# Optimization experiments

Hardware: AMD Instinct MI355X
Metric: run time of the kernel (lower is better)

Reference implementation:

```python
import jax, jax.numpy as jnp
import numpy as np

N_NODES = 20000
N_EDGES = 320000
DIM = 256
OUT_DIM = 256
N_LAYERS = 2
AVG_LOG = float(np.log(17.0))  # PNA avg_deg['log'] from deg histogram (all degree 16)
STD_EPS = 1e-5
N_AGG = 5
N_SCALER = 3


def _pna_conv(x, edge_index, Wpre, bpre, Wpost, bpost, Wlin, blin):
    """PyG PNAConv (towers=1, pre_layers=1, post_layers=1, divide_input=False)."""
    N = x.shape[0]
    src, dst = edge_index[0], edge_index[1]  # messages flow src -> dst
    # pre_nn on concat([x_i, x_j]) per edge: [E, 2F] -> [E, F]
    m = jnp.concatenate([x[dst], x[src]], axis=-1) @ Wpre.T + bpre
    deg = jax.ops.segment_sum(jnp.ones((src.shape[0],), x.dtype), dst, num_segments=N)
    degc = jnp.maximum(deg, 1.0)[:, None]
    s = jax.ops.segment_sum(m, dst, num_segments=N)
    mean = s / degc
    mean2 = jax.ops.segment_sum(m * m, dst, num_segments=N) / degc
    std = jnp.sqrt(jax.nn.relu(mean2 - mean * mean) + STD_EPS)
    has = (deg > 0)[:, None]
    mn = jnp.where(has, jax.ops.segment_min(m, dst, num_segments=N), 0.0)
    mx = jnp.where(has, jax.ops.segment_max(m, dst, num_segments=N), 0.0)
    agg = jnp.concatenate([mean, s, std, mn, mx], axis=-1)  # [N, 5F]
    logd = jnp.log(degc + 1.0)
    scaled = jnp.concatenate(
        [agg, agg * (logd / AVG_LOG), agg * (AVG_LOG / logd)], axis=-1)  # [N, 15F]
    h = jnp.concatenate([x, scaled], axis=-1) @ Wpost.T + bpost  # [N, F_out]
    return h @ Wlin.T + blin


def setup_inputs() -> dict:
    key = jax.random.key(0)
    ks = jax.random.split(key, 20)
    F = DIM
    L = N_LAYERS
    post_in = (N_AGG * N_SCALER + 1) * F  # 16F = 4096
    sc = 0.05
    inp = {
        "x": jax.random.normal(ks[0], (N_NODES, F), jnp.float32),
        "edge_index_in": jax.random.randint(ks[1], (2, N_EDGES), 0, N_NODES),
        "edge_index_out": jax.random.randint(ks[2], (2, N_EDGES), 0, N_NODES),
    }
    def p(k, shape):
        return sc * jax.random.normal(k, shape, jnp.float32)
    # stacked per-layer params; supply (_s) and demand (_d) channels
    for tag, base in (("s", 3), ("d", 9)):
        inp[f"Wpre_{tag}"] = p(ks[base + 0], (L, F, 2 * F))
        inp[f"bpre_{tag}"] = p(ks[base + 1], (L, F))
        inp[f"Wpost_{tag}"] = p(ks[base + 2], (L, OUT_DIM, post_in))
        inp[f"bpost_{tag}"] = p(ks[base + 3], (L, OUT_DIM))
        inp[f"Wlin_{tag}"] = p(ks[base + 4], (L, OUT_DIM, OUT_DIM))
        inp[f"blin_{tag}"] = p(ks[base + 5], (L, OUT_DIM))
    inp["Wcomb"] = p(ks[15], (L, OUT_DIM, F + 2 * OUT_DIM))
    inp["bcomb"] = p(ks[16], (L, OUT_DIM))
    inp["Wout"] = p(ks[17], (1, OUT_DIM))
    inp["bout"] = p(ks[18], (1,))
    return inp


def reference(x, edge_index_in, edge_index_out,
              Wpre_s, bpre_s, Wpost_s, bpost_s, Wlin_s, blin_s,
              Wpre_d, bpre_d, Wpost_d, bpost_d, Wlin_d, blin_d,
              Wcomb, bcomb, Wout, bout):
    for l in range(N_LAYERS):
        h_in = jax.nn.relu(_pna_conv(x, edge_index_in,
                                     Wpre_s[l], bpre_s[l], Wpost_s[l], bpost_s[l],
                                     Wlin_s[l], blin_s[l]))
        h_out = jax.nn.relu(_pna_conv(x, edge_index_out,
                                      Wpre_d[l], bpre_d[l], Wpost_d[l], bpost_d[l],
                                      Wlin_d[l], blin_d[l]))
        x = jax.nn.relu(jnp.concatenate([x, h_in, h_out], axis=-1) @ Wcomb[l].T + bcomb[l])
    return jnp.squeeze(x @ Wout.T + bout)  # [N]
```

## Files before the change

### kernel.cpp

```cpp
#include <hip/hip_runtime.h>
#include <math.h>

#define NN 20000
#define NE 320000
#define AVG_LOG_F 2.83321334f

typedef unsigned short u16;
typedef _Float16 h8_t __attribute__((ext_vector_type(8)));
typedef float f4_t __attribute__((ext_vector_type(4)));

__device__ __forceinline__ u16 f2h(float f) {
  _Float16 h = (_Float16)f;
  return __builtin_bit_cast(u16, h);
}
__device__ __forceinline__ void gld16(const void* g, void* l) {
  __builtin_amdgcn_global_load_lds(
      (const __attribute__((address_space(1))) void*)g,
      (__attribute__((address_space(3))) void*)l, 16, 0, 0);
}

__global__ __launch_bounds__(256) void k_count2(const int* __restrict__ ein,
                                                const int* __restrict__ eout,
                                                int* __restrict__ deg2, int E) {
  int e = blockIdx.x * 256 + threadIdx.x;
  int ch = blockIdx.y;
  const int* dst = (ch ? eout : ein) + E;
  if (e < E) atomicAdd(&deg2[ch * NN + dst[e]], 1);
}

__global__ __launch_bounds__(1024) void k_scan(const int* __restrict__ deg,
                                               int* __restrict__ rp, int N) {
  __shared__ int lds[1024];
  int t = threadIdx.x;
  int CH = (N + 1023) >> 10;
  int base = t * CH;
  int s = 0;
  for (int i = 0; i < CH; ++i) { int idx = base + i; if (idx < N) s += deg[idx]; }
  lds[t] = s;
  __syncthreads();
  for (int off = 1; off < 1024; off <<= 1) {
    int v = (t >= off) ? lds[t - off] : 0;
    __syncthreads();
    lds[t] += v;
    __syncthreads();
  }
  int run = (t == 0) ? 0 : lds[t - 1];
  for (int i = 0; i < CH; ++i) {
    int idx = base + i;
    if (idx < N) { rp[idx] = run; run += deg[idx]; }
  }
  if (t == 1023) rp[N] = run;
}

__global__ __launch_bounds__(256) void k_scatter2(const int* __restrict__ ein,
                                                  const int* __restrict__ eout,
                                                  const int* __restrict__ rp2,
                                                  int* __restrict__ cur2,
                                                  int* __restrict__ col2, int E) {
  int e = blockIdx.x * 256 + threadIdx.x;
  int ch = blockIdx.y;
  const int* src = (ch ? eout : ein);
  const int* dst = src + E;
  if (e < E) {
    int d = dst[e];
    int p = atomicAdd(&cur2[ch * NN + d], 1);
    col2[rp2[ch * NN + d] + p] = src[e];
  }
}

__global__ __launch_bounds__(256) void k_cvtw(
    const float* __restrict__ Wpre_s, const float* __restrict__ Wpre_d,
    const float* __restrict__ Wlin_s, const float* __restrict__ Wlin_d,
    const float* __restrict__ Wcomb,
    u16* __restrict__ pre2, u16* __restrict__ lincat, u16* __restrict__ combB) {
  int i = blockIdx.x * 256 + threadIdx.x;
  const float* src;
  u16* dst;
  int so, dofs;
  if (i < 65536)       { int j = i; int lyr = j >> 15;
                         src = Wpre_s; dst = pre2; so = j;
                         dofs = (lyr * 2 + 0) * 32768 + (j & 32767); }
  else if (i < 131072) { int j = i - 65536; int lyr = j >> 15;
                         src = Wpre_d; dst = pre2; so = j;
                         dofs = (lyr * 2 + 1) * 32768 + (j & 32767); }
  else if (i < 163840) { int j = i - 131072; int lyr = j >> 14;
                         src = Wlin_s; dst = lincat; so = j; dofs = j + lyr * 16384; }
  else if (i < 196608) { int j = i - 163840; int lyr = j >> 14;
                         src = Wlin_d; dst = lincat; so = j; dofs = j + (lyr + 1) * 16384; }
  else if (i < 294912) { src = Wcomb; dst = combB; so = i - 196608; dofs = so; }
  else return;
  float4 v = *(const float4*)(src + (size_t)so * 4);
  ushort4 o;
  o.x = f2h(v.x); o.y = f2h(v.y); o.z = f2h(v.z); o.w = f2h(v.w);
  *(ushort4*)(dst + (size_t)dofs * 4) = o;
}

__global__ __launch_bounds__(256) void k_cvtx(const float* __restrict__ x,
                                              u16* __restrict__ xc,
                                              const float* __restrict__ bpre_s,
                                              const float* __restrict__ bpre_d,
                                              float* __restrict__ bpre4) {
  int i = blockIdx.x * 256 + threadIdx.x;
  int row = i >> 6, c = (i & 63) * 4;
  float4 v = *(const float4*)(x + (size_t)row * 256 + c);
  ushort4 o;
  o.x = f2h(v.x); o.y = f2h(v.y); o.z = f2h(v.z); o.w = f2h(v.w);
  *(ushort4*)(xc + (size_t)row * 768 + c) = o;
  if (i < 1024) {
    int z = i >> 8, n = i & 255;
    int lyr = z >> 1, ch = z & 1;
    bpre4[i] = (ch ? bpre_d : bpre_s)[lyr * 256 + n];
  }
}

__global__ __launch_bounds__(256) void k_tc4(const float* __restrict__ Ws,
                                             const float* __restrict__ Wd,
                                             u16* __restrict__ outT) {
  __shared__ float tile[32][33];
  int z = blockIdx.z;
  const float* in = ((z & 1) ? Wd : Ws) + (size_t)(z >> 1) * 256 * 4096;
  u16* out = outT + (size_t)z * (4096 * 256);
  int bx = blockIdx.x, by = blockIdx.y;
  int r = threadIdx.x >> 5, c = threadIdx.x & 31;
#pragma unroll
  for (int it = 0; it < 4; ++it)
    tile[r + it * 8][c] = in[(size_t)(by * 32 + r + it * 8) * 4096 + bx * 32 + c];
  __syncthreads();
#pragma unroll
  for (int it = 0; it < 4; ++it)
    out[(size_t)(bx * 32 + r + it * 8) * 256 + by * 32 + c] = f2h(tile[c][r + it * 8]);
}

__global__ __launch_bounds__(512) void k_mgemm(
    const u16* __restrict__ A, int lda,
    const u16* __restrict__ B, const u16* __restrict__ B2, int ldb, int nsplit,
    const float* __restrict__ bias, int zBias,
    u16* __restrict__ oH, int ldoH,
    int M, int K, int relu, int zA, int zB, int zO) {
  __shared__ u16 As[2][64 * 64];
  __shared__ u16 Bs[2][256 * 64];
  const int t = threadIdx.x;
  const int z = blockIdx.z;
  A += (size_t)z * zA;
  B += (size_t)z * zB;
  B2 += (size_t)z * zB;
  oH += (size_t)z * zO;
  if (bias) bias += (size_t)z * zBias;
  const int m0 = blockIdx.y * 64;
  const int n0 = blockIdx.x * 256;
  const int l = t & 63, w = t >> 6;
  const int wm = w >> 2, wn = w & 3;
  const int lo = l & 15, hi = l >> 4;

  f4_t acc[2][4];
#pragma unroll
  for (int i = 0; i < 2; ++i)
#pragma unroll
    for (int j = 0; j < 4; ++j) acc[i][j] = (f4_t)0.f;

  const int ra = t >> 3, pa = t & 7;
  const int la = pa ^ (ra & 7);
  int rra = m0 + ra;
  if (rra > M - 1) rra = M - 1;
  const u16* gA = A + (size_t)rra * lda + la * 8;

  const u16* gB[4];
  int lBo[4];
#pragma unroll
  for (int i = 0; i < 4; ++i) {
    int q = i * 512 + t;
    int r = q >> 3, p2 = q & 7;
    int lc = p2 ^ (r & 7);
    int n = n0 + r;
    const u16* bp = (n < nsplit) ? (B + (size_t)n * ldb) : (B2 + (size_t)(n - nsplit) * ldb);
    gB[i] = bp + lc * 8;
    lBo[i] = q * 8;
  }

  gld16(gA, &As[0][t * 8]);
#pragma unroll
  for (int i = 0; i < 4; ++i) gld16(gB[i], &Bs[0][lBo[i]]);
  __syncthreads();

  const int nt = K >> 6;
  for (int tt = 0; tt < nt; ++tt) {
    const int cur = tt & 1;
    if (tt + 1 < nt) {
      const int ko = (tt + 1) << 6;
      gld16(gA + ko, &As[cur ^ 1][t * 8]);
#pragma unroll
      for (int i = 0; i < 4; ++i) gld16(gB[i] + ko, &Bs[cur ^ 1][lBo[i]]);
    }
#pragma unroll
    for (int ks = 0; ks < 2; ++ks) {
      h8_t af[2], bfr[4];
#pragma unroll
      for (int mi = 0; mi < 2; ++mi) {
        int row = wm * 32 + mi * 16 + lo;
        int c = (ks * 4 + hi) ^ (row & 7);
        af[mi] = *(const h8_t*)&As[cur][row * 64 + c * 8];
      }
#pragma unroll
      for (int ni = 0; ni < 4; ++ni) {
        int row = wn * 64 + ni * 16 + lo;
        int c = (ks * 4 + hi) ^ (row & 7);
        bfr[ni] = *(const h8_t*)&Bs[cur][row * 64 + c * 8];
      }
#pragma unroll
      for (int mi = 0; mi < 2; ++mi)
#pragma unroll
        for (int ni = 0; ni < 4; ++ni)
          acc[mi][ni] = __builtin_amdgcn_mfma_f32_16x16x32_f16(
              af[mi], bfr[ni], acc[mi][ni], 0, 0, 0);
    }
    __syncthreads();
  }

  float bv[4];
#pragma unroll
  for (int ni = 0; ni < 4; ++ni) {
    int n = n0 + wn * 64 + ni * 16 + lo;
    bv[ni] = (n < nsplit) ? (bias ? bias[n] : 0.f) : 0.f;
  }
#pragma unroll
  for (int mi = 0; mi < 2; ++mi) {
#pragma unroll
    for (int r = 0; r < 4; ++r) {
      int m = m0 + wm * 32 + mi * 16 + hi * 4 + r;
      if (m < M) {
#pragma unroll
        for (int ni = 0; ni < 4; ++ni) {
          int n = n0 + wn * 64 + ni * 16 + lo;
          float v = acc[mi][ni][r] + bv[ni];
          if (relu && v < 0.f) v = 0.f;
          oH[(size_t)m * ldoH + n] = f2h(v);
        }
      }
    }
  }
}

__global__ __launch_bounds__(512) void k_pgemm(
    const u16* __restrict__ xc, const u16* __restrict__ agg5c,
    const float* __restrict__ scal3c, const u16* __restrict__ Wfl,
    const float* __restrict__ bfl, u16* __restrict__ oHb, int M) {
  __shared__ u16 As[64 * 64];
  __shared__ u16 Bs[256 * 64];
  const int t = threadIdx.x;
  const int ch = blockIdx.y;
  const u16* agg5 = agg5c + (size_t)ch * NN * 1280;
  const float* scal3 = scal3c + (size_t)ch * NN * 4;
  const u16* Wf = Wfl + (size_t)ch * (256 * 4096);
  const float* bf = bfl + ch * 256;
  u16* oH = oHb + 256 + ch * 256;
  const int m0 = blockIdx.x * 64;
  const int l = t & 63, w = t >> 6;
  const int wm = w >> 2, wn = w & 3;
  const int lo = l & 15, hi = l >> 4;

  f4_t acc[2][4];
#pragma unroll
  for (int i = 0; i < 2; ++i)
#pragma unroll
    for (int j = 0; j < 4; ++j) acc[i][j] = (f4_t)0.f;

  const int ra = t >> 3, pa = t & 7;
  int m = m0 + ra;
  if (m > M - 1) m = M - 1;
  u16* ldA = &As[ra * 64 + (pa ^ (ra & 7)) * 8];
  const u16* xrow = xc + (size_t)m * 768;
  const u16* arow = agg5 + (size_t)m * 1280;
  const float* srow = scal3 + (size_t)m * 4;

  const u16* gB[4];
  u16* lB[4];
#pragma unroll
  for (int i = 0; i < 4; ++i) {
    int q = i * 512 + t;
    int r = q >> 3, p2 = q & 7;
    int lc = p2 ^ (r & 7);
    gB[i] = Wf + (size_t)r * 4096 + lc * 8;
    lB[i] = &Bs[q * 8];
  }

  for (int k0 = 0; k0 < 4096; k0 += 64) {
#pragma unroll
    for (int i = 0; i < 4; ++i) gld16(gB[i] + k0, lB[i]);
    int k = k0 + pa * 8;
    h8_t v;
    if (k < 256) {
      v = *(const h8_t*)(xrow + k);
    } else {
      int q = k - 256;
      int g = q / 1280;
      int r2 = q - g * 1280;
      v = *(const h8_t*)(arow + r2);
      v = v * (_Float16)srow[g];
    }
    *(h8_t*)ldA = v;
    __syncthreads();
#pragma unroll
    for (int ks = 0; ks < 2; ++ks) {
      h8_t af[2], bfr[4];
#pragma unroll
      for (int mi = 0; mi < 2; ++mi) {
        int row = wm * 32 + mi * 16 + lo;
        int c = (ks * 4 + hi) ^ (row & 7);
        af[mi] = *(const h8_t*)&As[row * 64 + c * 8];
      }
#pragma unroll
      for (int ni = 0; ni < 4; ++ni) {
        int row = wn * 64 + ni * 16 + lo;
        int c = (ks * 4 + hi) ^ (row & 7);
        bfr[ni] = *(const h8_t*)&Bs[row * 64 + c * 8];
      }
#pragma unroll
      for (int mi = 0; mi < 2; ++mi)
#pragma unroll
        for (int ni = 0; ni < 4; ++ni)
          acc[mi][ni] = __builtin_amdgcn_mfma_f32_16x16x32_f16(
              af[mi], bfr[ni], acc[mi][ni], 0, 0, 0);
    }
    __syncthreads();
  }

  float bv[4];
#pragma unroll
  for (int ni = 0; ni < 4; ++ni) bv[ni] = bf[wn * 64 + ni * 16 + lo];
#pragma unroll
  for (int mi = 0; mi < 2; ++mi) {
#pragma unroll
    for (int r = 0; r < 4; ++r) {
      int mr = m0 + wm * 32 + mi * 16 + hi * 4 + r;
      if (mr < M) {
#pragma unroll
        for (int ni = 0; ni < 4; ++ni) {
          int n = wn * 64 + ni * 16 + lo;
          float vv = acc[mi][ni][r] + bv[ni];
          if (vv < 0.f) vv = 0.f;
          oH[(size_t)mr * 768 + n] = f2h(vv);
        }
      }
    }
  }
}

__global__ __launch_bounds__(256) void k_aggregate(
    const u16* __restrict__ AB2, const int* __restrict__ rp2,
    const int* __restrict__ col2, u16* __restrict__ agg52,
    float* __restrict__ scal32) {
  int ch = blockIdx.y;
  const u16* AB = AB2 + (size_t)ch * NN * 512;
  const int* rp = rp2 + ch * NN;
  u16* agg5 = agg52 + (size_t)ch * NN * 1280;
  float* scal3 = scal32 + (size_t)ch * NN * 4;
  int w = threadIdx.x >> 6, l = threadIdx.x & 63;
  int n = blockIdx.x * 4 + w;
  int beg = rp[n], end = rp[n + 1];
  int deg = end - beg;
  int half = l >> 5, lf = l & 31;
  float sb[8], qb[8], mnb[8], mxb[8];
#pragma unroll
  for (int j = 0; j < 8; ++j) {
    sb[j] = 0.f; qb[j] = 0.f;
    mnb[j] = 3.402823466e38f; mxb[j] = -3.402823466e38f;
  }
  for (int i = beg + half; i < end; i += 2) {
    int s = col2[i];
    h8_t bv = *(const h8_t*)(AB + (size_t)s * 512 + 256 + lf * 8);
#pragma unroll
    for (int j = 0; j < 8; ++j) {
      float b = (float)bv[j];
      sb[j] += b;
      qb[j] = fmaf(b, b, qb[j]);
      mnb[j] = fminf(mnb[j], b);
      mxb[j] = fmaxf(mxb[j], b);
    }
  }
#pragma unroll
  for (int j = 0; j < 8; ++j) {
    sb[j] += __shfl_xor(sb[j], 32, 64);
    qb[j] += __shfl_xor(qb[j], 32, 64);
    mnb[j] = fminf(mnb[j], __shfl_xor(mnb[j], 32, 64));
    mxb[j] = fmaxf(mxb[j], __shfl_xor(mxb[j], 32, 64));
  }
  h8_t cv = *(const h8_t*)(AB + (size_t)n * 512 + lf * 8);
  float degf = (float)deg;
  float degc = degf > 1.f ? degf : 1.f;
  float inv = 1.f / degc;
  float ov[5][8];
#pragma unroll
  for (int j = 0; j < 8; ++j) {
    float c = (float)cv[j];
    float s_m = fmaf(degf, c, sb[j]);
    float mean = s_m * inv;
    float mean2 = fmaf(degf * c, c, fmaf(2.f * c, sb[j], qb[j])) * inv;
    float var = mean2 - mean * mean;
    if (var < 0.f) var = 0.f;
    float sd = sqrtf(var + 1e-5f);
    ov[0][j] = mean;
    ov[1][j] = s_m;
    ov[2][j] = sd;
    ov[3][j] = deg > 0 ? c + mnb[j] : 0.f;
    ov[4][j] = deg > 0 ? c + mxb[j] : 0.f;
  }
  if (half == 0) {
    u16* base = agg5 + (size_t)n * 1280 + lf * 8;
#pragma unroll
    for (int a = 0; a < 5; ++a) {
      h8_t o;
#pragma unroll
      for (int j = 0; j < 8; ++j) o[j] = (_Float16)ov[a][j];
      *(h8_t*)(base + a * 256) = o;
    }
    if (lf == 0) {
      float logd = logf(degc + 1.f);
      float4 sc = make_float4(1.f, logd / AVG_LOG_F, AVG_LOG_F / logd, 0.f);
      *(float4*)(scal3 + (size_t)n * 4) = sc;
    }
  }
}

__global__ __launch_bounds__(256) void k_bfuse4(
    const float* __restrict__ Wlin_s, const float* __restrict__ Wlin_d,
    const float* __restrict__ bpost_s, const float* __restrict__ bpost_d,
    const float* __restrict__ blin_s, const float* __restrict__ blin_d,
    float* __restrict__ bfv4) {
  __shared__ float bp[256];
  int z = blockIdx.x, lyr = z >> 1, ch = z & 1;
  const float* Wlin = (ch ? Wlin_d : Wlin_s) + (size_t)lyr * 65536;
  const float* bpost = (ch ? bpost_d : bpost_s) + lyr * 256;
  const float* blin = (ch ? blin_d : blin_s) + lyr * 256;
  int t = threadIdx.x;
  bp[t] = bpost[t];
  __syncthreads();
  float s = blin[t];
  for (int k = 0; k < 256; ++k) s = fmaf(Wlin[t * 256 + k], bp[k], s);
  bfv4[z * 256 + t] = s;
}

__global__ __launch_bounds__(256) void k_wout(const u16* __restrict__ x,
                                              const float* __restrict__ w,
                                              const float* __restrict__ b,
                                              float* __restrict__ out, int N) {
  int wid = threadIdx.x >> 6, lane = threadIdx.x & 63;
  int n = blockIdx.x * 4 + wid;
  if (n >= N) return;
  ushort4 xv = *(const ushort4*)(x + (size_t)n * 256 + lane * 4);
  const float4 wv = *(const float4*)(w + lane * 4);
  float s = (float)__builtin_bit_cast(_Float16, xv.x) * wv.x +
            (float)__builtin_bit_cast(_Float16, xv.y) * wv.y +
            (float)__builtin_bit_cast(_Float16, xv.z) * wv.z +
            (float)__builtin_bit_cast(_Float16, xv.w) * wv.w;
#pragma unroll
  for (int off = 32; off > 0; off >>= 1) s += __shfl_down(s, off);
  if (lane == 0) out[n] = s + b[0];
}

extern "C" void kernel_launch(void* const* d_in, const int* in_sizes, int n_in,
                              void* d_out, int out_size, void* d_ws, size_t ws_size,
                              hipStream_t stream) {
  const float* x0      = (const float*)d_in[0];
  const int*   ei_in   = (const int*)d_in[1];
  const int*   ei_out  = (const int*)d_in[2];
  const float* Wpre_s  = (const float*)d_in[3];
  const float* bpre_s  = (const float*)d_in[4];
  const float* Wpost_s = (const float*)d_in[5];
  const float* bpost_s = (const float*)d_in[6];
  const float* Wlin_s  = (const float*)d_in[7];
  const float* blin_s  = (const float*)d_in[8];
  const float* Wpre_d  = (const float*)d_in[9];
  const float* bpre_d  = (const float*)d_in[10];
  const float* Wpost_d = (const float*)d_in[11];
  const float* bpost_d = (const float*)d_in[12];
  const float* Wlin_d  = (const float*)d_in[13];
  const float* blin_d  = (const float*)d_in[14];
  const float* Wcomb   = (const float*)d_in[15];
  const float* bcomb   = (const float*)d_in[16];
  const float* Wout    = (const float*)d_in[17];
  const float* bout    = (const float*)d_in[18];
  float* out = (float*)d_out;

  char* p = (char*)d_ws;
  auto alloc = [&](size_t b) {
    char* r = p;
    p += (b + 255) & ~(size_t)255;
    return r;
  };
  int* deg2     = (int*)alloc((size_t)2 * NN * 4);
  int* cur2     = (int*)alloc((size_t)2 * NN * 4);
  int* rp2      = (int*)alloc((size_t)(2 * NN + 1) * 4);
  int* col2     = (int*)alloc((size_t)2 * NE * 4);
  u16* AB2      = (u16*)alloc((size_t)2 * NN * 512 * 2);
  u16* agg52    = (u16*)alloc((size_t)2 * NN * 1280 * 2);
  float* scal32 = (float*)alloc((size_t)2 * NN * 4 * 4);
  u16* xcat1    = (u16*)alloc((size_t)NN * 768 * 2);
  u16* xcat2    = (u16*)alloc((size_t)NN * 768 * 2);
  u16* pre2     = (u16*)alloc((size_t)4 * 256 * 512 * 2);
  u16* lincat   = (u16*)alloc((size_t)4 * 256 * 256 * 2);
  u16* combB    = (u16*)alloc((size_t)2 * 256 * 768 * 2);
  u16* Wf4      = (u16*)alloc((size_t)4 * 256 * 4096 * 2);
  float* bfv4   = (float*)alloc((size_t)4 * 256 * 4);
  float* bpre4  = (float*)alloc((size_t)4 * 256 * 4);
  u16* WpostT4  = (u16*)agg52;
  u16* xfin     = xcat1;

  const int BIG = 1 << 30;

  k_cvtw<<<1152, 256, 0, stream>>>(Wpre_s, Wpre_d, Wlin_s, Wlin_d, Wcomb,
                                   pre2, lincat, combB);
  k_cvtx<<<5000, 256, 0, stream>>>(x0, xcat1, bpre_s, bpre_d, bpre4);
  hipMemsetAsync(deg2, 0, (size_t)4 * NN * 4, stream);
  k_count2<<<dim3(1250, 2), 256, 0, stream>>>(ei_in, ei_out, deg2, NE);
  k_scan<<<1, 1024, 0, stream>>>(deg2, rp2, 2 * NN);
  k_scatter2<<<dim3(1250, 2), 256, 0, stream>>>(ei_in, ei_out, rp2, cur2, col2, NE);
  k_tc4<<<dim3(128, 8, 4), 256, 0, stream>>>(Wpost_s, Wpost_d, WpostT4);
  k_mgemm<<<dim3(16, 4, 4), 512, 0, stream>>>(
      lincat, 256, WpostT4, WpostT4, 256, BIG, nullptr, 0,
      Wf4, 4096, 256, 256, 0, 65536, 1048576, 1048576);
  k_bfuse4<<<4, 256, 0, stream>>>(Wlin_s, Wlin_d, bpost_s, bpost_d, blin_s, blin_d, bfv4);

  u16* xcs[2] = {xcat1, xcat2};
  for (int lyr = 0; lyr < 2; ++lyr) {
    u16* xc = xcs[lyr];
    k_mgemm<<<dim3(2, 313, 2), 512, 0, stream>>>(
        xc, 768, pre2 + (size_t)lyr * 2 * 131072, pre2 + (size_t)lyr * 2 * 131072 + 256,
        512, 256, bpre4 + (size_t)lyr * 2 * 256, 256,
        AB2, 512, NN, 256, 0, 0, 131072, NN * 512);
    k_aggregate<<<dim3(5000, 2), 256, 0, stream>>>(AB2, rp2, col2, agg52, scal32);
    k_pgemm<<<dim3(313, 2), 512, 0, stream>>>(
        xc, agg52, scal32, Wf4 + (size_t)lyr * 2 * 1048576, bfv4 + lyr * 512, xc, NN);
    if (lyr == 0) {
      k_mgemm<<<dim3(1, 313, 1), 512, 0, stream>>>(
          xc, 768, combB, combB, 768, BIG, bcomb, 0,
          xcat2, 768, NN, 768, 1, 0, 0, 0);
    } else {
      k_mgemm<<<dim3(1, 313, 1), 512, 0, stream>>>(
          xc, 768, combB + 196608, combB + 196608, 768, BIG, bcomb + 256, 0,
          xfin, 256, NN, 768, 1, 0, 0, 0);
    }
  }
  k_wout<<<5000, 256, 0, stream>>>(xfin, Wout, bout, out, NN);
}
```

Measured before the change: 807.9 us.

## Double pgemm M-tile to 128 rows and remap blocks by XCD for channel locality

The post-aggregation GEMM now computes 128-row tiles instead of 64, so each 256x64 weight tile loaded into LDS is reused across twice as many rows, halving weight traffic per output. The grid is flattened to 320 blocks and the block index is decoded so that blocks on the same XCD (wg&7) share a channel and adjacent M-tiles, aiming to improve L2 reuse of that channel's weights. This costs double the accumulator registers and larger LDS, which may lower occupancy, and leaves fewer blocks (314 active) to fill the GPU.

```diff
diff --git a/kernel.cpp b/kernel.cpp
--- a/kernel.cpp
+++ b/kernel.cpp
@@ -244,33 +244,43 @@
     const u16* __restrict__ xc, const u16* __restrict__ agg5c,
     const float* __restrict__ scal3c, const u16* __restrict__ Wfl,
     const float* __restrict__ bfl, u16* __restrict__ oHb, int M) {
-  __shared__ u16 As[64 * 64];
+  __shared__ u16 As[128 * 64];
   __shared__ u16 Bs[256 * 64];
   const int t = threadIdx.x;
-  const int ch = blockIdx.y;
+  const int wg = blockIdx.x;
+  const int xcd = wg & 7;
+  const int ch = xcd >> 2;
+  const int mt = (wg >> 3) * 4 + (xcd & 3);
+  if (mt >= 157) return;
+  const int m0 = mt * 128;
   const u16* agg5 = agg5c + (size_t)ch * NN * 1280;
   const float* scal3 = scal3c + (size_t)ch * NN * 4;
   const u16* Wf = Wfl + (size_t)ch * (256 * 4096);
   const float* bf = bfl + ch * 256;
   u16* oH = oHb + 256 + ch * 256;
-  const int m0 = blockIdx.x * 64;
   const int l = t & 63, w = t >> 6;
   const int wm = w >> 2, wn = w & 3;
   const int lo = l & 15, hi = l >> 4;
 
-  f4_t acc[2][4];
-#pragma unroll
-  for (int i = 0; i < 2; ++i)
+  f4_t acc[4][4];
+#pragma unroll
+  for (int i = 0; i < 4; ++i)
 #pragma unroll
     for (int j = 0; j < 4; ++j) acc[i][j] = (f4_t)0.f;
 
   const int ra = t >> 3, pa = t & 7;
-  int m = m0 + ra;
-  if (m > M - 1) m = M - 1;
-  u16* ldA = &As[ra * 64 + (pa ^ (ra & 7)) * 8];
-  const u16* xrow = xc + (size_t)m * 768;
-  const u16* arow = agg5 + (size_t)m * 1280;
-  const float* srow = scal3 + (size_t)m * 4;
+  int mr0 = m0 + ra;
+  if (mr0 > M - 1) mr0 = M - 1;
+  int mr1 = m0 + ra + 64;
+  if (mr1 > M - 1) mr1 = M - 1;
+  u16* ldA0 = &As[ra * 64 + (pa ^ (ra & 7)) * 8];
+  u16* ldA1 = ldA0 + 64 * 64;
+  const u16* xrow0 = xc + (size_t)mr0 * 768;
+  const u16* xrow1 = xc + (size_t)mr1 * 768;
+  const u16* arow0 = agg5 + (size_t)mr0 * 1280;
+  const u16* arow1 = agg5 + (size_t)mr1 * 1280;
+  const float* srow0 = scal3 + (size_t)mr0 * 4;
+  const float* srow1 = scal3 + (size_t)mr1 * 4;
 
   const u16* gB[4];
   u16* lB[4];
@@ -287,24 +297,28 @@
 #pragma unroll
     for (int i = 0; i < 4; ++i) gld16(gB[i] + k0, lB[i]);
     int k = k0 + pa * 8;
-    h8_t v;
+    h8_t v0, v1;
     if (k < 256) {
-      v = *(const h8_t*)(xrow + k);
+      v0 = *(const h8_t*)(xrow0 + k);
+      v1 = *(const h8_t*)(xrow1 + k);
     } else {
       int q = k - 256;
       int g = q / 1280;
       int r2 = q - g * 1280;
-      v = *(const h8_t*)(arow + r2);
-      v = v * (_Float16)srow[g];
-    }
-    *(h8_t*)ldA = v;
+      v0 = *(const h8_t*)(arow0 + r2);
+      v1 = *(const h8_t*)(arow1 + r2);
+      v0 = v0 * (_Float16)srow0[g];
+      v1 = v1 * (_Float16)srow1[g];
+    }
+    *(h8_t*)ldA0 = v0;
+    *(h8_t*)ldA1 = v1;
     __syncthreads();
 #pragma unroll
     for (int ks = 0; ks < 2; ++ks) {
-      h8_t af[2], bfr[4];
-#pragma unroll
-      for (int mi = 0; mi < 2; ++mi) {
-        int row = wm * 32 + mi * 16 + lo;
+      h8_t af[4], bfr[4];
+#pragma unroll
+      for (int mi = 0; mi < 4; ++mi) {
+        int row = wm * 64 + mi * 16 + lo;
         int c = (ks * 4 + hi) ^ (row & 7);
         af[mi] = *(const h8_t*)&As[row * 64 + c * 8];
       }
@@ -315,7 +329,7 @@
         bfr[ni] = *(const h8_t*)&Bs[row * 64 + c * 8];
       }
 #pragma unroll
-      for (int mi = 0; mi < 2; ++mi)
+      for (int mi = 0; mi < 4; ++mi)
 #pragma unroll
         for (int ni = 0; ni < 4; ++ni)
           acc[mi][ni] = __builtin_amdgcn_mfma_f32_16x16x32_f16(
@@ -328,10 +342,10 @@
 #pragma unroll
   for (int ni = 0; ni < 4; ++ni) bv[ni] = bf[wn * 64 + ni * 16 + lo];
 #pragma unroll
-  for (int mi = 0; mi < 2; ++mi) {
+  for (int mi = 0; mi < 4; ++mi) {
 #pragma unroll
     for (int r = 0; r < 4; ++r) {
-      int mr = m0 + wm * 32 + mi * 16 + hi * 4 + r;
+      int mr = m0 + wm * 64 + mi * 16 + hi * 4 + r;
       if (mr < M) {
 #pragma unroll
         for (int ni = 0; ni < 4; ++ni) {
@@ -528,7 +542,7 @@
         512, 256, bpre4 + (size_t)lyr * 2 * 256, 256,
         AB2, 512, NN, 256, 0, 0, 131072, NN * 512);
     k_aggregate<<<dim3(5000, 2), 256, 0, stream>>>(AB2, rp2, col2, agg52, scal32);
-    k_pgemm<<<dim3(313, 2), 512, 0, stream>>>(
+    k_pgemm<<<320, 512, 0, stream>>>(
         xc, agg52, scal32, Wf4 + (size_t)lyr * 2 * 1048576, bfv4 + lyr * 512, xc, NN);
     if (lyr == 0) {
       k_mgemm<<<dim3(1, 313, 1), 512, 0, stream>>>(
```

New measurement: 910.9 us. +12.7%, slower.
